# Kernel optimization log

Measured on AMD Instinct MI355X. Metric: run time of the kernel, lower is better.

Reference implementation:

```python
import jax, jax.numpy as jnp
import numpy as np

D_MODEL = 512
N_HEADS = 8
D_K = D_MODEL // N_HEADS
LN_EPS = 1e-5


def setup_inputs() -> dict:
    key = jax.random.key(0)
    ks = jax.random.split(key, 12)
    B, S = 2, 2048
    sc = 1.0 / np.sqrt(D_MODEL)
    inp = {
        'q': jax.random.normal(ks[0], (B, S, D_MODEL), jnp.float32),
        'k': jax.random.normal(ks[1], (B, S, D_MODEL), jnp.float32),
        'v': jax.random.normal(ks[2], (B, S, D_MODEL), jnp.float32),
        'Wq': jax.random.normal(ks[3], (D_MODEL, D_MODEL), jnp.float32) * sc,
        'bq': jnp.zeros((D_MODEL,), jnp.float32),
        'Wk': jax.random.normal(ks[4], (D_MODEL, D_MODEL), jnp.float32) * sc,
        'bk': jnp.zeros((D_MODEL,), jnp.float32),
        'Wv': jax.random.normal(ks[5], (D_MODEL, D_MODEL), jnp.float32) * sc,
        'bv': jnp.zeros((D_MODEL,), jnp.float32),
        'Wo': jax.random.normal(ks[6], (D_MODEL, D_MODEL), jnp.float32) * sc,
        'bo': jnp.zeros((D_MODEL,), jnp.float32),
        'gamma': jnp.ones((D_MODEL,), jnp.float32),
        'beta': jnp.zeros((D_MODEL,), jnp.float32),
    }
    return inp


def _split_heads(x):
    B, S, _ = x.shape
    return x.reshape(B, S, N_HEADS, D_K).transpose(0, 2, 1, 3)  # [B,H,S,d_k]


def reference(q, k, v, Wq, bq, Wk, bk, Wv, bv, Wo, bo, gamma, beta):
    B, S, _ = q.shape
    Q = _split_heads(q @ Wq.T + bq)
    K = _split_heads(k @ Wk.T + bk)
    V = _split_heads(v @ Wv.T + bv)
    scores = jnp.einsum('bhqd,bhkd->bhqk', Q, K) / jnp.sqrt(jnp.float32(D_K))
    attn = jax.nn.softmax(scores, axis=-1)  # [B,H,S,S]
    out = jnp.einsum('bhqk,bhkd->bhqd', attn, V)
    out = out.transpose(0, 2, 1, 3).reshape(B, S, D_MODEL)
    out = out @ Wo.T + bo
    x = out + q  # residual
    mu = jnp.mean(x, axis=-1, keepdims=True)
    var = jnp.mean(jnp.square(x - mu), axis=-1, keepdims=True)
    y = (x - mu) * jax.lax.rsqrt(var + LN_EPS) * gamma + beta
    return (y, attn)
```

## Files before the change

kernel.cpp:

```cpp
#include <hip/hip_runtime.h>
#include <hip/hip_bf16.h>

typedef __attribute__((ext_vector_type(8))) short short8;
typedef __attribute__((ext_vector_type(4))) short short4v;
typedef __attribute__((ext_vector_type(4))) float f32x4;

#define MFMA16(A, B, C) __builtin_amdgcn_mfma_f32_16x16x32_bf16(A, B, C, 0, 0, 0)

#define SEQ 2048
#define DM 512
#define NH 8
#define DK 64
#define NROWS 4096
#define NSPLIT 2
#define KBS (SEQ / NSPLIT)
#define NT (KBS / 64)

__device__ __forceinline__ short f2bf(float f) {
  union { float f; unsigned u; } x; x.f = f;
  unsigned r = (x.u + 0x7fffu + ((x.u >> 16) & 1u)) >> 16;
  return (short)r;
}
__device__ __forceinline__ float bf2f(short s) {
  union { unsigned u; float f; } x; x.u = ((unsigned)(unsigned short)s) << 16;
  return x.f;
}

__global__ __launch_bounds__(256) void cast3_kernel(
    const float* __restrict__ a, const float* __restrict__ b, const float* __restrict__ c,
    short* __restrict__ ab, short* __restrict__ bb, short* __restrict__ cb)
{
  int z = blockIdx.z;
  const float* src = (z == 0) ? a : (z == 1) ? b : c;
  short* dst = (z == 0) ? ab : (z == 1) ? bb : cb;
  size_t i = ((size_t)blockIdx.x * 256 + threadIdx.x) * 8;
  float4 f0 = *(const float4*)(src + i);
  float4 f1 = *(const float4*)(src + i + 4);
  short8 s;
  s[0] = f2bf(f0.x); s[1] = f2bf(f0.y); s[2] = f2bf(f0.z); s[3] = f2bf(f0.w);
  s[4] = f2bf(f1.x); s[5] = f2bf(f1.y); s[6] = f2bf(f1.z); s[7] = f2bf(f1.w);
  *(short8*)(dst + i) = s;
}

__global__ __launch_bounds__(256) void cast4_kernel(
    const float* __restrict__ a, const float* __restrict__ b,
    const float* __restrict__ c, const float* __restrict__ d,
    short* __restrict__ ab, short* __restrict__ bb,
    short* __restrict__ cb, short* __restrict__ db)
{
  int z = blockIdx.z;
  const float* src = (z == 0) ? a : (z == 1) ? b : (z == 2) ? c : d;
  short* dst = (z == 0) ? ab : (z == 1) ? bb : (z == 2) ? cb : db;
  size_t i = ((size_t)blockIdx.x * 256 + threadIdx.x) * 8;
  float4 f0 = *(const float4*)(src + i);
  float4 f1 = *(const float4*)(src + i + 4);
  short8 s;
  s[0] = f2bf(f0.x); s[1] = f2bf(f0.y); s[2] = f2bf(f0.z); s[3] = f2bf(f0.w);
  s[4] = f2bf(f1.x); s[5] = f2bf(f1.y); s[6] = f2bf(f1.z); s[7] = f2bf(f1.w);
  *(short8*)(dst + i) = s;
}

__global__ __launch_bounds__(256) void qkv_proj_kernel(
    const short* __restrict__ qbf, const short* __restrict__ kbf, const short* __restrict__ vbf,
    const short* __restrict__ Wqb, const short* __restrict__ Wkb, const short* __restrict__ Wvb,
    const float* __restrict__ bq, const float* __restrict__ bk, const float* __restrict__ bv,
    short* __restrict__ Qb, short* __restrict__ Kb, short* __restrict__ Vtb)
{
  int z = blockIdx.z;
  const short* X    = (z == 0) ? qbf : (z == 1) ? kbf : vbf;
  const short* W    = (z == 0) ? Wqb : (z == 1) ? Wkb : Wvb;
  const float* bias = (z == 0) ? bq  : (z == 1) ? bk  : bv;

  __shared__ short As[64][40];
  __shared__ short Bs[64][40];

  int t = threadIdx.x;
  int lane = t & 63, wave = t >> 6;
  int wr = wave >> 1, wc = wave & 1;
  int fr = lane & 15, fg = lane >> 4;
  int m0 = blockIdx.x * 64, n0 = blockIdx.y * 64;
  int lrow = t >> 2, lcol = (t & 3) * 8;

  f32x4 acc[2][2] = {};

  short8 a_pf = *(const short8*)(X + (size_t)(m0 + lrow) * DM + lcol);
  short8 b_pf = *(const short8*)(W + (size_t)(n0 + lrow) * DM + lcol);

  for (int k0 = 0; k0 < DM; k0 += 32) {
    __syncthreads();
    *(short8*)&As[lrow][lcol] = a_pf;
    *(short8*)&Bs[lrow][lcol] = b_pf;
    __syncthreads();
    if (k0 + 32 < DM) {
      a_pf = *(const short8*)(X + (size_t)(m0 + lrow) * DM + k0 + 32 + lcol);
      b_pf = *(const short8*)(W + (size_t)(n0 + lrow) * DM + k0 + 32 + lcol);
    }
    short8 a0 = *(const short8*)&As[wr * 32 + fr][fg * 8];
    short8 a1 = *(const short8*)&As[wr * 32 + 16 + fr][fg * 8];
    short8 b0 = *(const short8*)&Bs[wc * 32 + fr][fg * 8];
    short8 b1 = *(const short8*)&Bs[wc * 32 + 16 + fr][fg * 8];
    acc[0][0] = MFMA16(a0, b0, acc[0][0]);
    acc[0][1] = MFMA16(a0, b1, acc[0][1]);
    acc[1][0] = MFMA16(a1, b0, acc[1][0]);
    acc[1][1] = MFMA16(a1, b1, acc[1][1]);
  }

#pragma unroll
  for (int mi = 0; mi < 2; mi++)
#pragma unroll
    for (int ni = 0; ni < 2; ni++)
#pragma unroll
      for (int r = 0; r < 4; r++) {
        int row = m0 + wr * 32 + mi * 16 + fg * 4 + r;
        int col = n0 + wc * 32 + ni * 16 + fr;
        float val = acc[mi][ni][r] + bias[col];
        int bb = row >> 11, s = row & 2047, h = col >> 6, dk = col & 63;
        short o = f2bf(val);
        if (z == 0)      Qb[((size_t)(bb * NH + h) * SEQ + s) * DK + dk] = o;
        else if (z == 1) Kb[((size_t)(bb * NH + h) * SEQ + s) * DK + dk] = o;
        else             Vtb[((size_t)(bb * NH + h) * DK + dk) * SEQ + s] = o;
      }
}

__global__ __launch_bounds__(256) void den_kernel(
    const short* __restrict__ Q, const short* __restrict__ K, float* __restrict__ dp)
{
  __shared__ short Ks[64][72];

  int t = threadIdx.x, lane = t & 63, wave = t >> 6;
  int fr = lane & 15, fg = lane >> 4;
  int bh = blockIdx.y, z = blockIdx.z;
  const short* Qh = Q + (size_t)bh * SEQ * DK;
  const short* Kh = K + (size_t)bh * SEQ * DK;
  int q0 = blockIdx.x * 64 + wave * 16;

  short8 qa0 = *(const short8*)(Qh + (q0 + fr) * DK + fg * 8);
  short8 qa1 = *(const short8*)(Qh + (q0 + fr) * DK + 32 + fg * 8);

  int r_st = t >> 2, c_st = (t & 3) * 16;

  const short* kp0 = Kh + (size_t)(z * KBS + r_st) * DK + c_st;
  short8 k_pf0 = *(const short8*)kp0;
  short8 k_pf1 = *(const short8*)(kp0 + 8);

  float esum[4] = {0.f, 0.f, 0.f, 0.f};

  for (int kt = 0; kt < NT; kt++) {
    __syncthreads();
    *(short8*)&Ks[r_st][c_st]     = k_pf0;
    *(short8*)&Ks[r_st][c_st + 8] = k_pf1;
    __syncthreads();
    if (kt + 1 < NT) {
      const short* kp = Kh + (size_t)(z * KBS + (kt + 1) * 64 + r_st) * DK + c_st;
      k_pf0 = *(const short8*)kp;
      k_pf1 = *(const short8*)(kp + 8);
    }
#pragma unroll
    for (int ct = 0; ct < 4; ct++) {
      short8 k0v = *(const short8*)&Ks[ct * 16 + fr][fg * 8];
      short8 k1v = *(const short8*)&Ks[ct * 16 + fr][32 + fg * 8];
      f32x4 zz = {0.f, 0.f, 0.f, 0.f};
      zz = MFMA16(qa0, k0v, zz);
      zz = MFMA16(qa1, k1v, zz);
#pragma unroll
      for (int r = 0; r < 4; r++)
        esum[r] += __expf(zz[r] * 0.125f);
    }
  }

#pragma unroll
  for (int r = 0; r < 4; r++) {
    float e = esum[r];
    e += __shfl_xor(e, 1);
    e += __shfl_xor(e, 2);
    e += __shfl_xor(e, 4);
    e += __shfl_xor(e, 8);
    if (fr == 0)
      dp[((size_t)z * 16 + bh) * SEQ + q0 + fg * 4 + r] = e;
  }
}

__global__ __launch_bounds__(256) void attn_pv_kernel(
    const short* __restrict__ Q, const short* __restrict__ K, const short* __restrict__ Vt,
    const float* __restrict__ dp, float* __restrict__ attn, short* __restrict__ ctxp)
{
  __shared__ short Ks[64][72];
  __shared__ short Vs[64][72];
  __shared__ short P[4][16][72];

  int t = threadIdx.x, lane = t & 63, wave = t >> 6;
  int fr = lane & 15, fg = lane >> 4;
  int bh = blockIdx.y, z = blockIdx.z;
  const short* Qh = Q + (size_t)bh * SEQ * DK;
  const short* Kh = K + (size_t)bh * SEQ * DK;
  const short* Vh = Vt + (size_t)bh * DK * SEQ;
  int q0 = blockIdx.x * 64 + wave * 16;

  short8 qa0 = *(const short8*)(Qh + (q0 + fr) * DK + fg * 8);
  short8 qa1 = *(const short8*)(Qh + (q0 + fr) * DK + 32 + fg * 8);

  float rden[4];
#pragma unroll
  for (int r = 0; r < 4; r++) {
    int row = q0 + fg * 4 + r;
    float d = dp[((size_t)0 * 16 + bh) * SEQ + row] + dp[((size_t)1 * 16 + bh) * SEQ + row];
    rden[r] = 1.f / d;
  }

  int r_st = t >> 2, c_st = (t & 3) * 16;
  int rlo = lane >> 4, c4 = (lane & 15) * 4;

  f32x4 oacc[4] = {};

  const short* kp0 = Kh + (size_t)(z * KBS + r_st) * DK + c_st;
  const short* vp0 = Vh + (size_t)r_st * SEQ + z * KBS + c_st;
  short8 k_pf0 = *(const short8*)kp0;
  short8 k_pf1 = *(const short8*)(kp0 + 8);
  short8 v_pf0 = *(const short8*)vp0;
  short8 v_pf1 = *(const short8*)(vp0 + 8);

  for (int kt = 0; kt < NT; kt++) {
    int kb = z * KBS + kt * 64;
    __syncthreads();
    *(short8*)&Ks[r_st][c_st]     = k_pf0;
    *(short8*)&Ks[r_st][c_st + 8] = k_pf1;
    *(short8*)&Vs[r_st][c_st]     = v_pf0;
    *(short8*)&Vs[r_st][c_st + 8] = v_pf1;
    __syncthreads();
    if (kt + 1 < NT) {
      const short* kp = Kh + (size_t)(kb + 64 + r_st) * DK + c_st;
      const short* vp = Vh + (size_t)r_st * SEQ + kb + 64 + c_st;
      k_pf0 = *(const short8*)kp;
      k_pf1 = *(const short8*)(kp + 8);
      v_pf0 = *(const short8*)vp;
      v_pf1 = *(const short8*)(vp + 8);
    }

    f32x4 sc[4];
#pragma unroll
    for (int ct = 0; ct < 4; ct++) {
      short8 k0v = *(const short8*)&Ks[ct * 16 + fr][fg * 8];
      short8 k1v = *(const short8*)&Ks[ct * 16 + fr][32 + fg * 8];
      f32x4 zz = {0.f, 0.f, 0.f, 0.f};
      zz = MFMA16(qa0, k0v, zz);
      zz = MFMA16(qa1, k1v, zz);
      sc[ct] = zz;
    }

#pragma unroll
    for (int ct = 0; ct < 4; ct++)
#pragma unroll
      for (int r = 0; r < 4; r++) {
        float p = __expf(sc[ct][r] * 0.125f) * rden[r];
        P[wave][fg * 4 + r][ct * 16 + fr] = f2bf(p);
      }
    asm volatile("s_waitcnt lgkmcnt(0)" ::: "memory");

#pragma unroll
    for (int jr = 0; jr < 4; jr++) {
      int row = jr * 4 + rlo;
      short4v pv4 = *(const short4v*)&P[wave][row][c4];
      f32x4 vv = {bf2f(pv4[0]), bf2f(pv4[1]), bf2f(pv4[2]), bf2f(pv4[3])};
      __builtin_nontemporal_store(vv,
          (f32x4*)&attn[((size_t)(bh * SEQ + q0 + row)) * SEQ + kb + c4]);
    }

    short8 pa0 = *(const short8*)&P[wave][fr][fg * 8];
    short8 pa1 = *(const short8*)&P[wave][fr][32 + fg * 8];
#pragma unroll
    for (int dt = 0; dt < 4; dt++) {
      short8 v0 = *(const short8*)&Vs[dt * 16 + fr][fg * 8];
      short8 v1 = *(const short8*)&Vs[dt * 16 + fr][32 + fg * 8];
      oacc[dt] = MFMA16(pa0, v0, oacc[dt]);
      oacc[dt] = MFMA16(pa1, v1, oacc[dt]);
    }
  }

  int b = bh >> 3, h = bh & 7;
#pragma unroll
  for (int dt = 0; dt < 4; dt++)
#pragma unroll
    for (int r = 0; r < 4; r++) {
      int row = q0 + fg * 4 + r;
      ctxp[((size_t)z * NROWS + (size_t)b * SEQ + row) * DM + h * 64 + dt * 16 + fr] =
          f2bf(oacc[dt][r]);
    }
}

__global__ __launch_bounds__(256) void oproj_kernel(
    const short* __restrict__ ctxp, const short* __restrict__ Wob,
    const float* __restrict__ bias, const float* __restrict__ resid,
    float* __restrict__ xout)
{
  const size_t NPART = (size_t)NROWS * DM;
  __shared__ short As[64][40];
  __shared__ short Bs[64][40];

  int t = threadIdx.x;
  int lane = t & 63, wave = t >> 6;
  int wr = wave >> 1, wc = wave & 1;
  int fr = lane & 15, fg = lane >> 4;
  int m0 = blockIdx.x * 64, n0 = blockIdx.y * 64;
  int lrow = t >> 2, lcol = (t & 3) * 8;

  f32x4 acc[2][2] = {};

  size_t ia0 = (size_t)(m0 + lrow) * DM + lcol;
  short8 a_pf0 = *(const short8*)(ctxp + ia0);
  short8 a_pf1 = *(const short8*)(ctxp + NPART + ia0);
  short8 b_pf = *(const short8*)(Wob + (size_t)(n0 + lrow) * DM + lcol);

  for (int k0 = 0; k0 < DM; k0 += 32) {
    __syncthreads();
    {
      short8 sv;
#pragma unroll
      for (int j = 0; j < 8; j++)
        sv[j] = f2bf(bf2f(a_pf0[j]) + bf2f(a_pf1[j]));
      *(short8*)&As[lrow][lcol] = sv;
      *(short8*)&Bs[lrow][lcol] = b_pf;
    }
    __syncthreads();
    if (k0 + 32 < DM) {
      size_t ia = (size_t)(m0 + lrow) * DM + k0 + 32 + lcol;
      a_pf0 = *(const short8*)(ctxp + ia);
      a_pf1 = *(const short8*)(ctxp + NPART + ia);
      b_pf = *(const short8*)(Wob + (size_t)(n0 + lrow) * DM + k0 + 32 + lcol);
    }
    short8 a0 = *(const short8*)&As[wr * 32 + fr][fg * 8];
    short8 a1 = *(const short8*)&As[wr * 32 + 16 + fr][fg * 8];
    short8 b0 = *(const short8*)&Bs[wc * 32 + fr][fg * 8];
    short8 b1 = *(const short8*)&Bs[wc * 32 + 16 + fr][fg * 8];
    acc[0][0] = MFMA16(a0, b0, acc[0][0]);
    acc[0][1] = MFMA16(a0, b1, acc[0][1]);
    acc[1][0] = MFMA16(a1, b0, acc[1][0]);
    acc[1][1] = MFMA16(a1, b1, acc[1][1]);
  }

#pragma unroll
  for (int mi = 0; mi < 2; mi++)
#pragma unroll
    for (int ni = 0; ni < 2; ni++)
#pragma unroll
      for (int r = 0; r < 4; r++) {
        int row = m0 + wr * 32 + mi * 16 + fg * 4 + r;
        int col = n0 + wc * 32 + ni * 16 + fr;
        float val = acc[mi][ni][r] + bias[col] + resid[(size_t)row * DM + col];
        xout[(size_t)row * DM + col] = val;
      }
}

__global__ __launch_bounds__(256) void ln_kernel(
    const float* __restrict__ x, const float* __restrict__ gamma,
    const float* __restrict__ beta, float* __restrict__ y)
{
  int row = blockIdx.x * 4 + (threadIdx.x >> 6);
  int lane = threadIdx.x & 63;
  const float4* xr = (const float4*)(x + (size_t)row * DM);
  float4 v0 = xr[lane * 2];
  float4 v1 = xr[lane * 2 + 1];
  float s = v0.x + v0.y + v0.z + v0.w + v1.x + v1.y + v1.z + v1.w;
#pragma unroll
  for (int off = 1; off < 64; off <<= 1) s += __shfl_xor(s, off);
  float mean = s * (1.0f / DM);
  float a0 = v0.x - mean, a1 = v0.y - mean, a2 = v0.z - mean, a3 = v0.w - mean;
  float a4 = v1.x - mean, a5 = v1.y - mean, a6 = v1.z - mean, a7 = v1.w - mean;
  float vs = a0 * a0 + a1 * a1 + a2 * a2 + a3 * a3 + a4 * a4 + a5 * a5 + a6 * a6 + a7 * a7;
#pragma unroll
  for (int off = 1; off < 64; off <<= 1) vs += __shfl_xor(vs, off);
  float rstd = rsqrtf(vs * (1.0f / DM) + 1e-5f);
  const float4* gp = (const float4*)gamma;
  const float4* bp = (const float4*)beta;
  float4 g0 = gp[lane * 2], g1 = gp[lane * 2 + 1];
  float4 b0 = bp[lane * 2], b1 = bp[lane * 2 + 1];
  float4 o0, o1;
  o0.x = a0 * rstd * g0.x + b0.x; o0.y = a1 * rstd * g0.y + b0.y;
  o0.z = a2 * rstd * g0.z + b0.z; o0.w = a3 * rstd * g0.w + b0.w;
  o1.x = a4 * rstd * g1.x + b1.x; o1.y = a5 * rstd * g1.y + b1.y;
  o1.z = a6 * rstd * g1.z + b1.z; o1.w = a7 * rstd * g1.w + b1.w;
  float4* yr = (float4*)(y + (size_t)row * DM);
  yr[lane * 2] = o0;
  yr[lane * 2 + 1] = o1;
}

extern "C" void kernel_launch(void* const* d_in, const int* in_sizes, int n_in,
                              void* d_out, int out_size, void* d_ws, size_t ws_size,
                              hipStream_t stream)
{
  const float* q     = (const float*)d_in[0];
  const float* k     = (const float*)d_in[1];
  const float* v     = (const float*)d_in[2];
  const float* Wq    = (const float*)d_in[3];
  const float* bq    = (const float*)d_in[4];
  const float* Wk    = (const float*)d_in[5];
  const float* bk    = (const float*)d_in[6];
  const float* Wv    = (const float*)d_in[7];
  const float* bv    = (const float*)d_in[8];
  const float* Wo    = (const float*)d_in[9];
  const float* bo    = (const float*)d_in[10];
  const float* gamma = (const float*)d_in[11];
  const float* beta  = (const float*)d_in[12];

  char* w = (char*)d_ws;
  short* qbf  = (short*)(w);
  short* kbf  = (short*)(w + ((size_t)4  << 20));
  short* vbf  = (short*)(w + ((size_t)8  << 20));
  short* Qb   = (short*)(w + ((size_t)12 << 20));
  short* Kb   = (short*)(w + ((size_t)16 << 20));
  short* Vtb  = (short*)(w + ((size_t)20 << 20));
  short* Wqb  = (short*)(w + ((size_t)24 << 20));
  short* Wkb  = (short*)(w + ((size_t)24 << 20) + ((size_t)512 << 10));
  short* Wvb  = (short*)(w + ((size_t)25 << 20));
  short* Wob  = (short*)(w + ((size_t)25 << 20) + ((size_t)512 << 10));
  float* denp = (float*)(w + ((size_t)26 << 20));
  short* ctxp = (short*)(w);
  float* xbuf = (float*)(w + ((size_t)8 << 20));

  float* y = (float*)d_out;
  float* attnp = y + (size_t)NROWS * DM;

  cast3_kernel<<<dim3(1024, 1, 3), 256, 0, stream>>>(q, k, v, qbf, kbf, vbf);
  cast4_kernel<<<dim3(128, 1, 4), 256, 0, stream>>>(Wq, Wk, Wv, Wo, Wqb, Wkb, Wvb, Wob);
  qkv_proj_kernel<<<dim3(64, 8, 3), 256, 0, stream>>>(qbf, kbf, vbf, Wqb, Wkb, Wvb,
                                                      bq, bk, bv, Qb, Kb, Vtb);
  den_kernel<<<dim3(32, 16, NSPLIT), 256, 0, stream>>>(Qb, Kb, denp);
  attn_pv_kernel<<<dim3(32, 16, NSPLIT), 256, 0, stream>>>(Qb, Kb, Vtb, denp, attnp, ctxp);
  oproj_kernel<<<dim3(64, 8), 256, 0, stream>>>(ctxp, Wob, bo, q, xbuf);
  ln_kernel<<<1024, 256, 0, stream>>>(xbuf, gamma, beta, y);
}
```

Before: 143.3 us.

## Transpose score MFMA so each lane owns a query row; store attn directly

The operand order of the QK^T MFMA is swapped so each lane holds scores for a single query row. The attn matrix can then be written straight from registers as float4 non-temporal stores, with no bf16 round trip through LDS, and the denominator reduction needs only two cross-lane shuffles. The exp-and-multiply-by-reciprocal is folded into one exp2 with a log2-domain bias, and den_kernel's key split rises from 2 to 4 for more parallelism. In exchange, attn is now written in full fp32 precision, stores are 16-byte pieces spread across rows, and the reciprocal becomes a log followed by an exp2.

```diff
diff --git a/kernel.cpp b/kernel.cpp
--- a/kernel.cpp
+++ b/kernel.cpp
@@ -12,9 +12,11 @@
 #define NH 8
 #define DK 64
 #define NROWS 4096
-#define NSPLIT 2
-#define KBS (SEQ / NSPLIT)
-#define NT (KBS / 64)
+#define DSPLIT 4
+#define ASPLIT 2
+#define NT_D (SEQ / DSPLIT / 64)
+#define NT_A (SEQ / ASPLIT / 64)
+#define C1 0.180336880f
 
 __device__ __forceinline__ short f2bf(float f) {
   union { float f; unsigned u; } x; x.f = f;
@@ -133,25 +135,26 @@
   const short* Qh = Q + (size_t)bh * SEQ * DK;
   const short* Kh = K + (size_t)bh * SEQ * DK;
   int q0 = blockIdx.x * 64 + wave * 16;
+  const int kbase = z * (SEQ / DSPLIT);
 
   short8 qa0 = *(const short8*)(Qh + (q0 + fr) * DK + fg * 8);
   short8 qa1 = *(const short8*)(Qh + (q0 + fr) * DK + 32 + fg * 8);
 
   int r_st = t >> 2, c_st = (t & 3) * 16;
 
-  const short* kp0 = Kh + (size_t)(z * KBS + r_st) * DK + c_st;
+  const short* kp0 = Kh + (size_t)(kbase + r_st) * DK + c_st;
   short8 k_pf0 = *(const short8*)kp0;
   short8 k_pf1 = *(const short8*)(kp0 + 8);
 
-  float esum[4] = {0.f, 0.f, 0.f, 0.f};
-
-  for (int kt = 0; kt < NT; kt++) {
+  float esum = 0.f;
+
+  for (int kt = 0; kt < NT_D; kt++) {
     __syncthreads();
     *(short8*)&Ks[r_st][c_st]     = k_pf0;
     *(short8*)&Ks[r_st][c_st + 8] = k_pf1;
     __syncthreads();
-    if (kt + 1 < NT) {
-      const short* kp = Kh + (size_t)(z * KBS + (kt + 1) * 64 + r_st) * DK + c_st;
+    if (kt + 1 < NT_D) {
+      const short* kp = Kh + (size_t)(kbase + (kt + 1) * 64 + r_st) * DK + c_st;
       k_pf0 = *(const short8*)kp;
       k_pf1 = *(const short8*)(kp + 8);
     }
@@ -160,24 +163,18 @@
       short8 k0v = *(const short8*)&Ks[ct * 16 + fr][fg * 8];
       short8 k1v = *(const short8*)&Ks[ct * 16 + fr][32 + fg * 8];
       f32x4 zz = {0.f, 0.f, 0.f, 0.f};
-      zz = MFMA16(qa0, k0v, zz);
-      zz = MFMA16(qa1, k1v, zz);
+      zz = MFMA16(k0v, qa0, zz);
+      zz = MFMA16(k1v, qa1, zz);
 #pragma unroll
       for (int r = 0; r < 4; r++)
-        esum[r] += __expf(zz[r] * 0.125f);
+        esum += __builtin_amdgcn_exp2f(zz[r] * C1);
     }
   }
 
-#pragma unroll
-  for (int r = 0; r < 4; r++) {
-    float e = esum[r];
-    e += __shfl_xor(e, 1);
-    e += __shfl_xor(e, 2);
-    e += __shfl_xor(e, 4);
-    e += __shfl_xor(e, 8);
-    if (fr == 0)
-      dp[((size_t)z * 16 + bh) * SEQ + q0 + fg * 4 + r] = e;
-  }
+  esum += __shfl_xor(esum, 16);
+  esum += __shfl_xor(esum, 32);
+  if (lane < 16)
+    dp[((size_t)z * 16 + bh) * SEQ + q0 + lane] = esum;
 }
 
 __global__ __launch_bounds__(256) void attn_pv_kernel(
@@ -195,39 +192,37 @@
   const short* Kh = K + (size_t)bh * SEQ * DK;
   const short* Vh = Vt + (size_t)bh * DK * SEQ;
   int q0 = blockIdx.x * 64 + wave * 16;
+  const int kbase = z * (SEQ / ASPLIT);
 
   short8 qa0 = *(const short8*)(Qh + (q0 + fr) * DK + fg * 8);
   short8 qa1 = *(const short8*)(Qh + (q0 + fr) * DK + 32 + fg * 8);
 
-  float rden[4];
-#pragma unroll
-  for (int r = 0; r < 4; r++) {
-    int row = q0 + fg * 4 + r;
-    float d = dp[((size_t)0 * 16 + bh) * SEQ + row] + dp[((size_t)1 * 16 + bh) * SEQ + row];
-    rden[r] = 1.f / d;
-  }
+  float dsum = 0.f;
+#pragma unroll
+  for (int zz = 0; zz < DSPLIT; zz++)
+    dsum += dp[((size_t)zz * 16 + bh) * SEQ + q0 + fr];
+  float lg2r = -__builtin_amdgcn_logf(dsum);
 
   int r_st = t >> 2, c_st = (t & 3) * 16;
-  int rlo = lane >> 4, c4 = (lane & 15) * 4;
 
   f32x4 oacc[4] = {};
 
-  const short* kp0 = Kh + (size_t)(z * KBS + r_st) * DK + c_st;
-  const short* vp0 = Vh + (size_t)r_st * SEQ + z * KBS + c_st;
+  const short* kp0 = Kh + (size_t)(kbase + r_st) * DK + c_st;
+  const short* vp0 = Vh + (size_t)r_st * SEQ + kbase + c_st;
   short8 k_pf0 = *(const short8*)kp0;
   short8 k_pf1 = *(const short8*)(kp0 + 8);
   short8 v_pf0 = *(const short8*)vp0;
   short8 v_pf1 = *(const short8*)(vp0 + 8);
 
-  for (int kt = 0; kt < NT; kt++) {
-    int kb = z * KBS + kt * 64;
+  for (int kt = 0; kt < NT_A; kt++) {
+    int kb = kbase + kt * 64;
     __syncthreads();
     *(short8*)&Ks[r_st][c_st]     = k_pf0;
     *(short8*)&Ks[r_st][c_st + 8] = k_pf1;
     *(short8*)&Vs[r_st][c_st]     = v_pf0;
     *(short8*)&Vs[r_st][c_st + 8] = v_pf1;
     __syncthreads();
-    if (kt + 1 < NT) {
+    if (kt + 1 < NT_A) {
       const short* kp = Kh + (size_t)(kb + 64 + r_st) * DK + c_st;
       const short* vp = Vh + (size_t)r_st * SEQ + kb + 64 + c_st;
       k_pf0 = *(const short8*)kp;
@@ -236,34 +231,25 @@
       v_pf1 = *(const short8*)(vp + 8);
     }
 
-    f32x4 sc[4];
 #pragma unroll
     for (int ct = 0; ct < 4; ct++) {
       short8 k0v = *(const short8*)&Ks[ct * 16 + fr][fg * 8];
       short8 k1v = *(const short8*)&Ks[ct * 16 + fr][32 + fg * 8];
       f32x4 zz = {0.f, 0.f, 0.f, 0.f};
-      zz = MFMA16(qa0, k0v, zz);
-      zz = MFMA16(qa1, k1v, zz);
-      sc[ct] = zz;
-    }
-
-#pragma unroll
-    for (int ct = 0; ct < 4; ct++)
-#pragma unroll
-      for (int r = 0; r < 4; r++) {
-        float p = __expf(sc[ct][r] * 0.125f) * rden[r];
-        P[wave][fg * 4 + r][ct * 16 + fr] = f2bf(p);
-      }
+      zz = MFMA16(k0v, qa0, zz);
+      zz = MFMA16(k1v, qa1, zz);
+      f32x4 p;
+#pragma unroll
+      for (int r = 0; r < 4; r++)
+        p[r] = __builtin_amdgcn_exp2f(zz[r] * C1 + lg2r);
+      __builtin_nontemporal_store(p,
+          (f32x4*)&attn[((size_t)(bh * SEQ + q0 + fr)) * SEQ + kb + ct * 16 + fg * 4]);
+      short4v pk;
+#pragma unroll
+      for (int r = 0; r < 4; r++) pk[r] = f2bf(p[r]);
+      *(short4v*)&P[wave][fr][ct * 16 + fg * 4] = pk;
+    }
     asm volatile("s_waitcnt lgkmcnt(0)" ::: "memory");
-
-#pragma unroll
-    for (int jr = 0; jr < 4; jr++) {
-      int row = jr * 4 + rlo;
-      short4v pv4 = *(const short4v*)&P[wave][row][c4];
-      f32x4 vv = {bf2f(pv4[0]), bf2f(pv4[1]), bf2f(pv4[2]), bf2f(pv4[3])};
-      __builtin_nontemporal_store(vv,
-          (f32x4*)&attn[((size_t)(bh * SEQ + q0 + row)) * SEQ + kb + c4]);
-    }
 
     short8 pa0 = *(const short8*)&P[wave][fr][fg * 8];
     short8 pa1 = *(const short8*)&P[wave][fr][32 + fg * 8];
@@ -423,8 +409,8 @@
   cast4_kernel<<<dim3(128, 1, 4), 256, 0, stream>>>(Wq, Wk, Wv, Wo, Wqb, Wkb, Wvb, Wob);
   qkv_proj_kernel<<<dim3(64, 8, 3), 256, 0, stream>>>(qbf, kbf, vbf, Wqb, Wkb, Wvb,
                                                       bq, bk, bv, Qb, Kb, Vtb);
-  den_kernel<<<dim3(32, 16, NSPLIT), 256, 0, stream>>>(Qb, Kb, denp);
-  attn_pv_kernel<<<dim3(32, 16, NSPLIT), 256, 0, stream>>>(Qb, Kb, Vtb, denp, attnp, ctxp);
+  den_kernel<<<dim3(32, 16, DSPLIT), 256, 0, stream>>>(Qb, Kb, denp);
+  attn_pv_kernel<<<dim3(32, 16, ASPLIT), 256, 0, stream>>>(Qb, Kb, Vtb, denp, attnp, ctxp);
   oproj_kernel<<<dim3(64, 8), 256, 0, stream>>>(ctxp, Wob, bo, q, xbuf);
   ln_kernel<<<1024, 256, 0, stream>>>(xbuf, gamma, beta, y);
 }
```

Result: slower. 162.7 us (+13.5%).
